# Kernel tuning notes

Hardware: AMD Instinct MI355X
Metric: run time of the kernel (lower is better)

## Reference

```python
import jax, jax.numpy as jnp
import numpy as np

N_NODES = 100000
N_EDGES = 3200000
IN_DIM = 128
H1, F1 = 8, 8          # layer1: 8 heads x 8 feats -> concat 64
N_CLASSES = 40         # layer2: 1 head -> classes
NEG_SLOPE = 0.2        # GAT LeakyReLU slope


def setup_inputs() -> dict:
    key = jax.random.key(0)
    ks = jax.random.split(key, 8)
    x = jax.random.normal(ks[0], (N_NODES, IN_DIM), dtype=jnp.float32)
    adj = jax.random.randint(ks[1], (2, N_EDGES), 0, N_NODES, dtype=jnp.int64)
    s1 = 1.0 / np.sqrt(IN_DIM)
    s2 = 1.0 / np.sqrt(H1 * F1)
    W1 = jax.random.normal(ks[2], (IN_DIM, H1 * F1), dtype=jnp.float32) * s1
    a1_src = jax.random.normal(ks[3], (H1, F1), dtype=jnp.float32) * s2
    a1_dst = jax.random.normal(ks[4], (H1, F1), dtype=jnp.float32) * s2
    W2 = jax.random.normal(ks[5], (H1 * F1, N_CLASSES), dtype=jnp.float32) * s2
    a2_src = jax.random.normal(ks[6], (1, N_CLASSES), dtype=jnp.float32) * s2
    a2_dst = jax.random.normal(ks[7], (1, N_CLASSES), dtype=jnp.float32) * s2
    return {"input_matrix": x, "adjacency_coo_matrix": adj,
            "W1": W1, "a1_src": a1_src, "a1_dst": a1_dst,
            "W2": W2, "a2_src": a2_src, "a2_dst": a2_dst}


def gat_layer(x, src, dst, W, a_s, a_d, heads, fdim):
    n = x.shape[0]
    h = (x @ W).reshape(n, heads, fdim)                 # [N,H,F]
    e_src = jnp.sum(h * a_s, axis=-1)                   # [N,H]
    e_dst = jnp.sum(h * a_d, axis=-1)                   # [N,H]
    e = jax.nn.leaky_relu(e_src[src] + e_dst[dst], NEG_SLOPE)  # [E,H]
    m = jax.ops.segment_max(e, dst, num_segments=n)     # per-dst softmax max
    p = jnp.exp(e - m[dst])
    s = jax.ops.segment_sum(p, dst, num_segments=n)
    alpha = p / s[dst]                                  # [E,H]
    out = jax.ops.segment_sum(alpha[:, :, None] * h[src], dst, num_segments=n)
    return out                                          # [N,H,F]


def reference(input_matrix, adjacency_coo_matrix, W1, a1_src, a1_dst, W2, a2_src, a2_dst):
    n = input_matrix.shape[0]
    loops = jnp.arange(n, dtype=adjacency_coo_matrix.dtype)
    src = jnp.concatenate([adjacency_coo_matrix[0], loops])
    dst = jnp.concatenate([adjacency_coo_matrix[1], loops])
    x = gat_layer(input_matrix, src, dst, W1, a1_src, a1_dst, H1, F1)
    x = jax.nn.elu(x.reshape(n, H1 * F1))               # concat heads + ELU
    x = gat_layer(x, src, dst, W2, a2_src, a2_dst, 1, N_CLASSES)
    return jax.nn.log_softmax(x.reshape(n, N_CLASSES), axis=1)
```

## Files before the change

kernel.cpp:

```cpp
#include <hip/hip_runtime.h>
#include <hip/hip_fp16.h>
#include <math.h>

#define NN 100000
#define EE 3200000
#define ET (EE + NN)
#define BKW 128
#define NBK ((NN + BKW - 1) / BKW)
#define BCAP 5120
#define EPB 4096
#define NB_P1 ((EE + EPB - 1) / EPB)
#define NB_G 391

#define R1 80
#define R2 48

typedef float v2f __attribute__((ext_vector_type(2)));
typedef float v4f __attribute__((ext_vector_type(4)));
typedef _Float16 v8h __attribute__((ext_vector_type(8)));

__device__ __forceinline__ float lrelu(float v) { return fmaxf(v, 0.2f * v); }

__device__ __forceinline__ unsigned char to_fp8(float v) {
  return (unsigned char)(__builtin_amdgcn_cvt_pk_fp8_f32(v, v, 0, false) & 0xff);
}


__global__ __launch_bounds__(256) void k_p1(const int* __restrict__ srcs,
                                            const int* __restrict__ dsts,
                                            int* __restrict__ bcount,
                                            int* __restrict__ bbuf) {
  __shared__ int lcnt[NBK];
  __shared__ int lbase[NBK];
  int tid = threadIdx.x;
  for (int i = tid; i < NBK; i += 256) lcnt[i] = 0;
  __syncthreads();
  int e0 = blockIdx.x * EPB;
  int rank[16], bkt[16], pk[16];
#pragma unroll
  for (int i = 0; i < 16; ++i) {
    int e = e0 + tid + i * 256;
    bkt[i] = -1;
    if (e < EE) {
      int d = dsts[e];
      int s = srcs[e];
      int b = d >> 7;
      rank[i] = atomicAdd(&lcnt[b], 1);
      bkt[i] = b;
      pk[i] = (s << 7) | (d & 127);
    }
  }
  __syncthreads();
  for (int i = tid; i < NBK; i += 256) {
    int c = lcnt[i];
    lbase[i] = c ? atomicAdd(&bcount[i], c) : 0;
  }
  __syncthreads();
#pragma unroll
  for (int i = 0; i < 16; ++i) {
    if (bkt[i] >= 0) {
      bbuf[(size_t)bkt[i] * BCAP + lbase[bkt[i]] + rank[i]] = pk[i];
    }
  }
}

__global__ void k_bscan(const int* __restrict__ bcount, int* __restrict__ bbase) {
  __shared__ int s[1024];
  int t = threadIdx.x;
  int v = 0;
  if (t < NBK) v = bcount[t] + min(BKW, NN - (t << 7));
  s[t] = v;
  __syncthreads();
  for (int off = 1; off < 1024; off <<= 1) {
    int u = (t >= off) ? s[t - off] : 0;
    __syncthreads();
    s[t] += u;
    __syncthreads();
  }
  if (t < NBK) bbase[t] = s[t] - v;
}

__global__ __launch_bounds__(256) void k_p2(const int* __restrict__ bcount,
                                            const int* __restrict__ bbase,
                                            const int* __restrict__ bbuf,
                                            int* __restrict__ offsets,
                                            int* __restrict__ edge_src) {
  __shared__ int cnt[BKW];
  __shared__ int s1[BKW];
  __shared__ int cur[BKW];
  int b = blockIdx.x, tid = threadIdx.x;
  int d0 = b << 7;
  int width = min(BKW, NN - d0);
  int n = bcount[b];
  int base = bbase[b];
  const int* buf = bbuf + (size_t)b * BCAP;
  if (tid < BKW) cnt[tid] = (tid < width) ? 1 : 0;
  __syncthreads();
  for (int i = tid; i < n; i += 256) atomicAdd(&cnt[buf[i] & 127], 1);
  __syncthreads();
  if (tid < BKW) s1[tid] = cnt[tid];
  __syncthreads();
  for (int off = 1; off < BKW; off <<= 1) {
    int u = (tid < BKW && tid >= off) ? s1[tid - off] : 0;
    __syncthreads();
    if (tid < BKW) s1[tid] += u;
    __syncthreads();
  }
  if (tid < width) {
    int excl = s1[tid] - cnt[tid];
    offsets[d0 + tid] = base + excl;
    edge_src[base + excl] = d0 + tid;
    cur[tid] = excl + 1;
  }
  if (b == 0 && tid == 0) offsets[NN] = ET;
  __syncthreads();
  for (int i = tid; i < n; i += 256) {
    int p = buf[i];
    int pos = atomicAdd(&cur[p & 127], 1);
    edge_src[base + pos] = p >> 7;
  }
}


__global__ __launch_bounds__(256) void k_gemm1(
    const float* __restrict__ x, const float* __restrict__ W1,
    const float* __restrict__ a1s, const float* __restrict__ a1d,
    unsigned char* __restrict__ P1, float* __restrict__ ed1) {
  __shared__ _Float16 Wb[16 * 64 * 8];
  int tid = threadIdx.x;
  for (int idx = tid; idx < 16 * 64; idx += 256) {
    int f = idx >> 6, l = idx & 63;
    int nt = f >> 2, kk = f & 3;
    int ql = l >> 4, cl = l & 15;
    int col = nt * 16 + cl;
    int k0 = kk * 32 + ql * 8;
    v8h tmp;
#pragma unroll
    for (int j = 0; j < 8; ++j) tmp[j] = (_Float16)W1[(k0 + j) * 64 + col];
    *reinterpret_cast<v8h*>(&Wb[idx * 8]) = tmp;
  }
  __syncthreads();
  int wv = tid >> 6, lane = tid & 63;
  int q = lane >> 4, c = lane & 15;
  v8h bf[16];
#pragma unroll
  for (int f = 0; f < 16; ++f)
    bf[f] = *reinterpret_cast<const v8h*>(&Wb[(f * 64 + lane) * 8]);
  float a1s_l[4], a1d_l[4];
#pragma unroll
  for (int nt = 0; nt < 4; ++nt) {
    a1s_l[nt] = a1s[nt * 16 + c];
    a1d_l[nt] = a1d[nt * 16 + c];
  }
  for (int t = 0; t < 4; ++t) {
    int n0 = blockIdx.x * 256 + wv * 64 + t * 16;
    int row = n0 + c;
    row = (row < NN) ? row : (NN - 1);
    v4f acc[4] = {{0.f,0.f,0.f,0.f},{0.f,0.f,0.f,0.f},{0.f,0.f,0.f,0.f},{0.f,0.f,0.f,0.f}};
#pragma unroll
    for (int kk = 0; kk < 4; ++kk) {
      const float* xp = x + (size_t)row * 128 + kk * 32 + q * 8;
      float4 x0 = *reinterpret_cast<const float4*>(xp);
      float4 x1 = *reinterpret_cast<const float4*>(xp + 4);
      v8h af;
      af[0] = (_Float16)x0.x; af[1] = (_Float16)x0.y;
      af[2] = (_Float16)x0.z; af[3] = (_Float16)x0.w;
      af[4] = (_Float16)x1.x; af[5] = (_Float16)x1.y;
      af[6] = (_Float16)x1.z; af[7] = (_Float16)x1.w;
#pragma unroll
      for (int nt = 0; nt < 4; ++nt)
        acc[nt] = __builtin_amdgcn_mfma_f32_16x16x32_f16(af, bf[nt * 4 + kk], acc[nt], 0, 0, 0);
    }
#pragma unroll
    for (int nt = 0; nt < 4; ++nt) {
#pragma unroll
      for (int r = 0; r < 4; ++r) {
        float val = acc[nt][r];
        float vs = val * a1s_l[nt];
        float vd = val * a1d_l[nt];
        vs += __shfl_xor(vs, 1); vs += __shfl_xor(vs, 2); vs += __shfl_xor(vs, 4);
        vd += __shfl_xor(vd, 1); vd += __shfl_xor(vd, 2); vd += __shfl_xor(vd, 4);
        int node = n0 + q * 4 + r;
        if (node < NN) {
          unsigned char* rec = P1 + (size_t)node * R1;
          rec[16 + nt * 16 + c] = to_fp8(val);
          if ((c & 7) == 0) {
            int head = 2 * nt + (c >> 3);
            *reinterpret_cast<__half*>(rec + 2 * head) = __float2half(vs);
            ed1[node * 8 + head] = vd;
          }
        }
      }
    }
  }
}


__global__ __launch_bounds__(256) void k_agg1(
    const int* __restrict__ offsets, const int* __restrict__ edge_src,
    const unsigned char* __restrict__ P1, const float* __restrict__ ed1,
    __half* __restrict__ x2) {
  int wv = threadIdx.x >> 6, lane = threadIdx.x & 63;
  int g = lane >> 3, p = lane & 7;
  int dst = blockIdx.x * 32 + wv * 8 + g;
  float edv = ed1[dst * 8 + p];
  int beg = offsets[dst], end = offsets[dst + 1];
  int deg = end - beg;
  int md = deg;
#pragma unroll
  for (int o = 8; o < 64; o <<= 1) md = max(md, __shfl_xor(md, o, 64));
  float l = 0.f;
  float a[8] = {0.f, 0.f, 0.f, 0.f, 0.f, 0.f, 0.f, 0.f};
  for (int t = 0; t < md; t += 4) {
    int src[4]; uint2 raw[4]; float es[4]; float pr[4];
#pragma unroll
    for (int i = 0; i < 4; ++i) {
      int idx = t + i;
      int ci = beg + ((idx < deg) ? idx : (deg - 1));
      src[i] = edge_src[ci];
    }
#pragma unroll
    for (int i = 0; i < 4; ++i) {
      const unsigned char* rec = P1 + (size_t)src[i] * R1;
      es[i] = __half2float(*reinterpret_cast<const __half*>(rec + 2 * p));
      raw[i] = *reinterpret_cast<const uint2*>(rec + 16 + (p << 3));
    }
#pragma unroll
    for (int i = 0; i < 4; ++i) {
      float e = lrelu(es[i] + edv);
      pr[i] = (t + i < deg) ? __expf(e) : 0.f;
    }
#pragma unroll
    for (int i = 0; i < 4; ++i) {
      v2f f01 = __builtin_amdgcn_cvt_pk_f32_fp8(raw[i].x, false);
      v2f f23 = __builtin_amdgcn_cvt_pk_f32_fp8(raw[i].x, true);
      v2f f45 = __builtin_amdgcn_cvt_pk_f32_fp8(raw[i].y, false);
      v2f f67 = __builtin_amdgcn_cvt_pk_f32_fp8(raw[i].y, true);
      l += pr[i];
      a[0] += pr[i] * f01.x; a[1] += pr[i] * f01.y;
      a[2] += pr[i] * f23.x; a[3] += pr[i] * f23.y;
      a[4] += pr[i] * f45.x; a[5] += pr[i] * f45.y;
      a[6] += pr[i] * f67.x; a[7] += pr[i] * f67.y;
    }
  }
  float rl = 1.f / l;
  union { __half h[8]; uint4 u; } pk;
#pragma unroll
  for (int i = 0; i < 8; ++i) {
    float v = a[i] * rl;
    v = (v > 0.f) ? v : (__expf(v) - 1.f);
    pk.h[i] = __float2half(v);
  }
  *reinterpret_cast<uint4*>(x2 + ((size_t)dst << 6) + (p << 3)) = pk.u;
}


__global__ __launch_bounds__(256) void k_gemm2(
    const __half* __restrict__ x2, const float* __restrict__ W2,
    const float* __restrict__ a2s, const float* __restrict__ a2d,
    unsigned char* __restrict__ P2, float* __restrict__ ed2) {
  __shared__ _Float16 Wb[6 * 64 * 8];
  int tid = threadIdx.x;
  for (int idx = tid; idx < 6 * 64; idx += 256) {
    int f = idx >> 6, l = idx & 63;
    int nt = f >> 1, kk = f & 1;
    int ql = l >> 4, cl = l & 15;
    int col = nt * 16 + cl;
    int k0 = kk * 32 + ql * 8;
    v8h tmp;
#pragma unroll
    for (int j = 0; j < 8; ++j)
      tmp[j] = (col < 40) ? (_Float16)W2[(k0 + j) * 40 + col] : (_Float16)0.f;
    *reinterpret_cast<v8h*>(&Wb[idx * 8]) = tmp;
  }
  __syncthreads();
  int wv = tid >> 6, lane = tid & 63;
  int q = lane >> 4, c = lane & 15;
  v8h bf[6];
#pragma unroll
  for (int f = 0; f < 6; ++f)
    bf[f] = *reinterpret_cast<const v8h*>(&Wb[(f * 64 + lane) * 8]);
  float a2s_l[3], a2d_l[3];
#pragma unroll
  for (int nt = 0; nt < 3; ++nt) {
    int n = nt * 16 + c;
    a2s_l[nt] = (n < 40) ? a2s[n] : 0.f;
    a2d_l[nt] = (n < 40) ? a2d[n] : 0.f;
  }
  for (int t = 0; t < 4; ++t) {
    int n0 = blockIdx.x * 256 + wv * 64 + t * 16;
    int row = n0 + c;
    row = (row < NN) ? row : (NN - 1);
    v4f acc[3] = {{0.f,0.f,0.f,0.f},{0.f,0.f,0.f,0.f},{0.f,0.f,0.f,0.f}};
#pragma unroll
    for (int kk = 0; kk < 2; ++kk) {
      v8h af = *reinterpret_cast<const v8h*>(x2 + (size_t)row * 64 + kk * 32 + q * 8);
#pragma unroll
      for (int nt = 0; nt < 3; ++nt)
        acc[nt] = __builtin_amdgcn_mfma_f32_16x16x32_f16(af, bf[nt * 2 + kk], acc[nt], 0, 0, 0);
    }
#pragma unroll
    for (int r = 0; r < 4; ++r) {
      float v0 = acc[0][r], v1 = acc[1][r], v2 = acc[2][r];
      float s = v0 * a2s_l[0] + v1 * a2s_l[1] + v2 * a2s_l[2];
      float d = v0 * a2d_l[0] + v1 * a2d_l[1] + v2 * a2d_l[2];
      s += __shfl_xor(s, 1); s += __shfl_xor(s, 2); s += __shfl_xor(s, 4); s += __shfl_xor(s, 8);
      d += __shfl_xor(d, 1); d += __shfl_xor(d, 2); d += __shfl_xor(d, 4); d += __shfl_xor(d, 8);
      int node = n0 + q * 4 + r;
      if (node < NN) {
        unsigned char* rec = P2 + (size_t)node * R2;
        if (c < 8) rec[4 + 32 + c] = to_fp8(v2);
        rec[4 + c]      = to_fp8(v0);
        rec[4 + 16 + c] = to_fp8(v1);
        if (c == 0) {
          *reinterpret_cast<__half*>(rec) = __float2half(s);
          ed2[node] = d;
        }
      }
    }
  }
}


__global__ __launch_bounds__(256) void k_agg2(
    const int* __restrict__ offsets, const int* __restrict__ edge_src,
    const unsigned char* __restrict__ P2, const float* __restrict__ ed2,
    float* __restrict__ out) {
  int wv = threadIdx.x >> 6, lane = threadIdx.x & 63;
  int g = lane >> 4, p = lane & 15;
  bool act = p < 10;
  int cp = act ? p : 0;
  int dst = blockIdx.x * 16 + wv * 4 + g;
  float edv = ed2[dst];
  int beg = offsets[dst], end = offsets[dst + 1];
  int deg = end - beg;
  int md = deg;
#pragma unroll
  for (int o = 16; o < 64; o <<= 1) md = max(md, __shfl_xor(md, o, 64));
  float l = 0.f;
  float a[4] = {0.f, 0.f, 0.f, 0.f};
  for (int t = 0; t < md; t += 4) {
    int src[4]; unsigned raw[4]; float es[4]; float pr[4];
#pragma unroll
    for (int i = 0; i < 4; ++i) {
      int idx = t + i;
      int ci = beg + ((idx < deg) ? idx : (deg - 1));
      src[i] = edge_src[ci];
    }
#pragma unroll
    for (int i = 0; i < 4; ++i) {
      const unsigned char* rec = P2 + (size_t)src[i] * R2;
      es[i] = __half2float(*reinterpret_cast<const __half*>(rec));
      raw[i] = *reinterpret_cast<const unsigned*>(rec + 4 + (cp << 2));
    }
#pragma unroll
    for (int i = 0; i < 4; ++i) {
      float e = lrelu(es[i] + edv);
      pr[i] = (t + i < deg) ? __expf(e) : 0.f;
    }
#pragma unroll
    for (int i = 0; i < 4; ++i) {
      v2f f01 = __builtin_amdgcn_cvt_pk_f32_fp8(raw[i], false);
      v2f f23 = __builtin_amdgcn_cvt_pk_f32_fp8(raw[i], true);
      l += pr[i];
      a[0] += pr[i] * f01.x; a[1] += pr[i] * f01.y;
      a[2] += pr[i] * f23.x; a[3] += pr[i] * f23.y;
    }
  }
  float rl = 1.f / l;
  float v0 = a[0] * rl, v1 = a[1] * rl, v2 = a[2] * rl, v3 = a[3] * rl;
  float red = act ? fmaxf(fmaxf(v0, v1), fmaxf(v2, v3)) : -INFINITY;
#pragma unroll
  for (int o = 1; o < 16; o <<= 1) red = fmaxf(red, __shfl_xor(red, o, 64));
  float se = act ? (__expf(v0 - red) + __expf(v1 - red) + __expf(v2 - red) + __expf(v3 - red)) : 0.f;
#pragma unroll
  for (int o = 1; o < 16; o <<= 1) se += __shfl_xor(se, o, 64);
  float ls = red + __logf(se);
  if (act) {
    float4 o4 = make_float4(v0 - ls, v1 - ls, v2 - ls, v3 - ls);
    *reinterpret_cast<float4*>(out + (size_t)dst * 40 + (p << 2)) = o4;
  }
}


extern "C" void kernel_launch(void* const* d_in, const int* in_sizes, int n_in,
                              void* d_out, int out_size, void* d_ws, size_t ws_size,
                              hipStream_t stream) {
  const float* x   = (const float*)d_in[0];
  const int*   adj = (const int*)d_in[1];
  const float* W1  = (const float*)d_in[2];
  const float* a1s = (const float*)d_in[3];
  const float* a1d = (const float*)d_in[4];
  const float* W2  = (const float*)d_in[5];
  const float* a2s = (const float*)d_in[6];
  const float* a2d = (const float*)d_in[7];
  float* out = (float*)d_out;

  const int* srcs = adj;
  const int* dsts = adj + EE;

  char* w = (char*)d_ws;
  size_t off = 0;
  auto alloc = [&](size_t bytes) -> void* {
    void* p = w + off;
    off = (off + bytes + 255) & ~(size_t)255;
    return p;
  };
  int* offsets      = (int*)alloc((size_t)(NN + 1) * 4);
  int* edge_src     = (int*)alloc((size_t)ET * 4);
  int* bcount       = (int*)alloc((size_t)NBK * 4);
  int* bbase        = (int*)alloc((size_t)NBK * 4);
  unsigned char* P1 = (unsigned char*)alloc((size_t)NN * R1);
  float* ed1        = (float*)alloc((size_t)NN * 8 * 4);
  __half* x2        = (__half*)alloc((size_t)NN * 64 * 2);
  int* bbuf         = (int*)alloc((size_t)NBK * BCAP * 4);
  unsigned char* P2 = P1;
  float* ed2 = ed1;

  hipMemsetAsync(bcount, 0, (size_t)NBK * 4, stream);
  k_p1<<<NB_P1, 256, 0, stream>>>(srcs, dsts, bcount, bbuf);
  k_bscan<<<1, 1024, 0, stream>>>(bcount, bbase);
  k_p2<<<NBK, 256, 0, stream>>>(bcount, bbase, bbuf, offsets, edge_src);

  k_gemm1<<<NB_G, 256, 0, stream>>>(x, W1, a1s, a1d, P1, ed1);
  k_agg1<<<NN / 32, 256, 0, stream>>>(offsets, edge_src, P1, ed1, x2);
  k_gemm2<<<NB_G, 256, 0, stream>>>(x2, W2, a2s, a2d, P2, ed2);
  k_agg2<<<NN / 16, 256, 0, stream>>>(offsets, edge_src, P2, ed2, out);
}
```

Before: 332.5 us.

## Sort destination nodes by degree to balance per-wave work in aggregation

Adds a counting sort of nodes by in-degree (histogram, descending scan, scatter) producing a permutation. The aggregation kernels process destinations in this degree-sorted order, so the nodes sharing a wavefront have similar degrees and fewer lanes idle while waiting for the max-degree node. This costs three extra small kernel launches plus a memset, and it makes per-node reads and writes less sequential.

```diff
diff --git a/kernel.cpp b/kernel.cpp
--- a/kernel.cpp
+++ b/kernel.cpp
@@ -11,6 +11,7 @@
 #define EPB 4096
 #define NB_P1 ((EE + EPB - 1) / EPB)
 #define NB_G 391
+#define DBINS 512
 
 #define R1 80
 #define R2 48
@@ -118,6 +119,41 @@
     int p = buf[i];
     int pos = atomicAdd(&cur[p & 127], 1);
     edge_src[base + pos] = p >> 7;
+  }
+}
+
+
+__global__ void k_dhist(const int* __restrict__ offsets, int* __restrict__ dhist) {
+  int i = blockIdx.x * 256 + threadIdx.x;
+  if (i < NN) {
+    int deg = offsets[i + 1] - offsets[i];
+    atomicAdd(&dhist[min(deg, DBINS - 1)], 1);
+  }
+}
+
+__global__ void k_dscan(const int* __restrict__ dhist, int* __restrict__ dbase) {
+  __shared__ int s[DBINS];
+  int t = threadIdx.x;
+  int v = dhist[DBINS - 1 - t];
+  s[t] = v;
+  __syncthreads();
+  for (int off = 1; off < DBINS; off <<= 1) {
+    int u = (t >= off) ? s[t - off] : 0;
+    __syncthreads();
+    s[t] += u;
+    __syncthreads();
+  }
+  dbase[DBINS - 1 - t] = s[t] - v;
+}
+
+__global__ void k_dscatter(const int* __restrict__ offsets, const int* __restrict__ dbase,
+                           int* __restrict__ dcur, int* __restrict__ perm) {
+  int i = blockIdx.x * 256 + threadIdx.x;
+  if (i < NN) {
+    int deg = offsets[i + 1] - offsets[i];
+    int b = min(deg, DBINS - 1);
+    int pos = dbase[b] + atomicAdd(&dcur[b], 1);
+    perm[pos] = i;
   }
 }
 
@@ -198,11 +234,12 @@
 
 __global__ __launch_bounds__(256) void k_agg1(
     const int* __restrict__ offsets, const int* __restrict__ edge_src,
+    const int* __restrict__ perm,
     const unsigned char* __restrict__ P1, const float* __restrict__ ed1,
     __half* __restrict__ x2) {
   int wv = threadIdx.x >> 6, lane = threadIdx.x & 63;
   int g = lane >> 3, p = lane & 7;
-  int dst = blockIdx.x * 32 + wv * 8 + g;
+  int dst = perm[blockIdx.x * 32 + wv * 8 + g];
   float edv = ed1[dst * 8 + p];
   int beg = offsets[dst], end = offsets[dst + 1];
   int deg = end - beg;
@@ -324,13 +361,14 @@
 
 __global__ __launch_bounds__(256) void k_agg2(
     const int* __restrict__ offsets, const int* __restrict__ edge_src,
+    const int* __restrict__ perm,
     const unsigned char* __restrict__ P2, const float* __restrict__ ed2,
     float* __restrict__ out) {
   int wv = threadIdx.x >> 6, lane = threadIdx.x & 63;
   int g = lane >> 4, p = lane & 15;
   bool act = p < 10;
   int cp = act ? p : 0;
-  int dst = blockIdx.x * 16 + wv * 4 + g;
+  int dst = perm[blockIdx.x * 16 + wv * 4 + g];
   float edv = ed2[dst];
   int beg = offsets[dst], end = offsets[dst + 1];
   int deg = end - beg;
@@ -410,20 +448,30 @@
   int* edge_src     = (int*)alloc((size_t)ET * 4);
   int* bcount       = (int*)alloc((size_t)NBK * 4);
   int* bbase        = (int*)alloc((size_t)NBK * 4);
+  int* perm         = (int*)alloc((size_t)NN * 4);
+  int* dmeta        = (int*)alloc((size_t)3 * DBINS * 4);
   unsigned char* P1 = (unsigned char*)alloc((size_t)NN * R1);
   float* ed1        = (float*)alloc((size_t)NN * 8 * 4);
   __half* x2        = (__half*)alloc((size_t)NN * 64 * 2);
   int* bbuf         = (int*)alloc((size_t)NBK * BCAP * 4);
+  int* dhist = dmeta;
+  int* dbase = dmeta + DBINS;
+  int* dcur  = dmeta + 2 * DBINS;
   unsigned char* P2 = P1;
   float* ed2 = ed1;
 
   hipMemsetAsync(bcount, 0, (size_t)NBK * 4, stream);
+  hipMemsetAsync(dmeta, 0, (size_t)3 * DBINS * 4, stream);
   k_p1<<<NB_P1, 256, 0, stream>>>(srcs, dsts, bcount, bbuf);
   k_bscan<<<1, 1024, 0, stream>>>(bcount, bbase);
   k_p2<<<NBK, 256, 0, stream>>>(bcount, bbase, bbuf, offsets, edge_src);
 
+  k_dhist<<<NB_G, 256, 0, stream>>>(offsets, dhist);
+  k_dscan<<<1, DBINS, 0, stream>>>(dhist, dbase);
+  k_dscatter<<<NB_G, 256, 0, stream>>>(offsets, dbase, dcur, perm);
+
   k_gemm1<<<NB_G, 256, 0, stream>>>(x, W1, a1s, a1d, P1, ed1);
-  k_agg1<<<NN / 32, 256, 0, stream>>>(offsets, edge_src, P1, ed1, x2);
+  k_agg1<<<NN / 32, 256, 0, stream>>>(offsets, edge_src, perm, P1, ed1, x2);
   k_gemm2<<<NB_G, 256, 0, stream>>>(x2, W2, a2s, a2d, P2, ed2);
-  k_agg2<<<NN / 16, 256, 0, stream>>>(offsets, edge_src, P2, ed2, out);
-}
+  k_agg2<<<NN / 16, 256, 0, stream>>>(offsets, edge_src, perm, P2, ed2, out);
+}
```

After: 722.8 us. 2.17x slower.
